# Kernel optimization log

Hardware: AMD Instinct MI355X
Metric: run time of the kernel (lower is better)

Reference implementation:

```python
import jax, jax.numpy as jnp
import numpy as np

THETA = 10000.0


def _apply_rope(xh, positions, theta):
    # xh: [B, H, S, d_k]; positions: [S] int
    d_k = xh.shape[-1]
    inv_freq = theta ** (-jnp.arange(0, d_k, 2, dtype=jnp.float32) / d_k)  # [d_k/2]
    angles = positions.astype(jnp.float32)[:, None] * inv_freq[None, :]     # [S, d_k/2]
    cos = jnp.cos(angles)
    sin = jnp.sin(angles)
    x1 = xh[..., 0::2]
    x2 = xh[..., 1::2]
    r1 = x1 * cos - x2 * sin
    r2 = x1 * sin + x2 * cos
    return jnp.stack([r1, r2], axis=-1).reshape(xh.shape)


def setup_inputs() -> dict:
    key = jax.random.key(0)
    ks = jax.random.split(key, 5)
    B, S, D = 2, 2048, 1024
    std = np.sqrt(1.0 / D).astype(np.float32)
    return {
        "x": jax.random.normal(ks[0], (B, S, D), dtype=jnp.float32),
        "token_positions": jnp.arange(S, dtype=jnp.int64 if jax.config.jax_enable_x64 else jnp.int32),
        "Wq": jax.random.normal(ks[1], (D, D), dtype=jnp.float32) * std,
        "Wk": jax.random.normal(ks[2], (D, D), dtype=jnp.float32) * std,
        "Wv": jax.random.normal(ks[3], (D, D), dtype=jnp.float32) * std,
        "Wo": jax.random.normal(ks[4], (D, D), dtype=jnp.float32) * std,
    }


def reference(x, token_positions, Wq, Wk, Wv, Wo):
    B, S, D = x.shape
    n_heads = 16
    d_k = D // n_heads

    # QKV projections (torch does x @ W.T)
    q = x @ Wq.T
    k = x @ Wk.T
    v = x @ Wv.T

    def split_heads(t):  # [B,S,D] -> [B,H,S,d_k]
        return t.reshape(B, S, n_heads, d_k).transpose(0, 2, 1, 3)

    qh = _apply_rope(split_heads(q), token_positions, THETA)
    kh = _apply_rope(split_heads(k), token_positions, THETA)
    vh = split_heads(v)

    scores = jnp.einsum("bhqd,bhkd->bhqk", qh, kh) / jnp.sqrt(jnp.float32(d_k))
    causal = jnp.tril(jnp.ones((S, S), dtype=bool))
    scores = jnp.where(causal, scores, -jnp.inf)
    attn = jax.nn.softmax(scores, axis=-1)

    out_h = jnp.einsum("bhqk,bhkd->bhqd", attn, vh)  # [B,H,S,d_k]
    out = out_h.transpose(0, 2, 1, 3).reshape(B, S, D)
    return out @ Wo.T
```

## Files before the change

kernel.cpp:

```cpp
#include <hip/hip_runtime.h>

typedef unsigned int u32;
typedef __attribute__((ext_vector_type(8))) short short8;
typedef __attribute__((ext_vector_type(4))) float f32x4;

__device__ __forceinline__ unsigned short f2bf(float f) {
  union { float f; u32 u; } x; x.f = f;
  u32 u = x.u;
  return (unsigned short)((u + 0x7fffu + ((u >> 16) & 1u)) >> 16);
}
__device__ __forceinline__ float bf2f(unsigned short b) {
  union { u32 u; float f; } x; x.u = ((u32)b) << 16;
  return x.f;
}
__device__ __forceinline__ f32x4 mfma_bf16(short8 a, short8 b, f32x4 c) {
  return __builtin_amdgcn_mfma_f32_16x16x32_bf16(a, b, c, 0, 0, 0);
}

typedef __attribute__((address_space(3))) unsigned int lds_u32;
typedef const __attribute__((address_space(1))) unsigned int glb_u32;
__device__ __forceinline__ void gload_lds16(const unsigned short* g, unsigned short* l) {
  __builtin_amdgcn_global_load_lds((glb_u32*)g, (lds_u32*)l, 16, 0, 0);
}

__global__ __launch_bounds__(256) void cvt_kernel(const float* __restrict__ src,
                                                  unsigned short* __restrict__ dst, int n4) {
  int i = blockIdx.x * 256 + threadIdx.x;
  if (i >= n4) return;
  float4 v = ((const float4*)src)[i];
  ushort4 o;
  o.x = f2bf(v.x); o.y = f2bf(v.y); o.z = f2bf(v.z); o.w = f2bf(v.w);
  ((ushort4*)dst)[i] = o;
}

__global__ __launch_bounds__(256) void cvt_w_kernel(const float* __restrict__ wq,
                                                    const float* __restrict__ wk,
                                                    const float* __restrict__ wv,
                                                    const float* __restrict__ wo,
                                                    unsigned short* __restrict__ dqkv,
                                                    unsigned short* __restrict__ dwo) {
  const int i = blockIdx.x * 256 + threadIdx.x;
  const int w = blockIdx.y;
  const float* src = (w == 0) ? wq : (w == 1) ? wk : (w == 2) ? wv : wo;
  unsigned short* dst = (w == 3) ? dwo : dqkv + (size_t)w * 1048576;
  float4 v = ((const float4*)src)[i];
  ushort4 o;
  o.x = f2bf(v.x); o.y = f2bf(v.y); o.z = f2bf(v.z); o.w = f2bf(v.w);
  ((ushort4*)dst)[i] = o;
}

__global__ __launch_bounds__(256) void gemm_qkv(const unsigned short* __restrict__ A,
                                                const unsigned short* __restrict__ B,
                                                unsigned short* __restrict__ qk,
                                                unsigned short* __restrict__ kk,
                                                unsigned short* __restrict__ vtm) {
  constexpr int K = 1024;
  __shared__ unsigned short As[128 * 64];
  __shared__ unsigned short Bs[128 * 64];
  const int tid = threadIdx.x;
  const int wave = tid >> 6, lane = tid & 63;
  const int l15 = lane & 15, quad = lane >> 4;
  const int wr = wave >> 1, wc = wave & 1;
  const int m0 = blockIdx.y * 128, n0 = blockIdx.x * 128;
  f32x4 acc[4][4] = {};
  const int srow = wave * 32 + (lane >> 3);
  const int scol = (((lane & 7) ^ ((lane >> 3) & 7)) * 8);
  const unsigned short* Ag = A + (size_t)(m0 + srow) * K + scol;
  const unsigned short* Bg = B + (size_t)(n0 + srow) * K + scol;
  const int sw0 = ((0 + quad) ^ (l15 & 7)) * 8;
  const int sw1 = ((4 + quad) ^ (l15 & 7)) * 8;
  for (int k0 = 0; k0 < K; k0 += 64) {
    __syncthreads();
#pragma unroll
    for (int r = 0; r < 4; ++r) {
      gload_lds16(Ag + k0 + (size_t)(8 * r) * K, &As[(wave * 32 + 8 * r) * 64]);
      gload_lds16(Bg + k0 + (size_t)(8 * r) * K, &Bs[(wave * 32 + 8 * r) * 64]);
    }
    __syncthreads();
    short8 a[4][2], b[4][2];
#pragma unroll
    for (int i = 0; i < 4; ++i) {
      const int row = (wr * 64 + i * 16 + l15) * 64;
      a[i][0] = *(const short8*)&As[row + sw0];
      a[i][1] = *(const short8*)&As[row + sw1];
    }
#pragma unroll
    for (int j = 0; j < 4; ++j) {
      const int row = (wc * 64 + j * 16 + l15) * 64;
      b[j][0] = *(const short8*)&Bs[row + sw0];
      b[j][1] = *(const short8*)&Bs[row + sw1];
    }
#pragma unroll
    for (int i = 0; i < 4; ++i)
#pragma unroll
      for (int j = 0; j < 4; ++j) {
        acc[i][j] = mfma_bf16(a[i][0], b[j][0], acc[i][j]);
        acc[i][j] = mfma_bf16(a[i][1], b[j][1], acc[i][j]);
      }
  }
  const int proj = n0 >> 10;
  const int nn0 = (n0 & 1023) + wc * 64;
  if (proj < 2) {
    unsigned short* dst = (proj == 0) ? qk : kk;
#pragma unroll
    for (int i = 0; i < 4; ++i) {
      const int mb = m0 + wr * 64 + i * 16 + quad * 4;
#pragma unroll
      for (int j = 0; j < 4; ++j) {
        const int nn = nn0 + j * 16 + l15;
#pragma unroll
        for (int r = 0; r < 4; ++r) dst[(size_t)(mb + r) * 1024 + nn] = f2bf(acc[i][j][r]);
      }
    }
  } else {
#pragma unroll
    for (int i = 0; i < 4; ++i) {
      const int mb = m0 + wr * 64 + i * 16 + quad * 4;
      const int bb = mb >> 11, s = mb & 2047;
#pragma unroll
      for (int j = 0; j < 4; ++j) {
        const int nn = nn0 + j * 16 + l15;
        const int h = nn >> 6, d = nn & 63;
        ushort4 v4;
        v4.x = f2bf(acc[i][j][0]); v4.y = f2bf(acc[i][j][1]);
        v4.z = f2bf(acc[i][j][2]); v4.w = f2bf(acc[i][j][3]);
        *(ushort4*)&vtm[(((size_t)bb * 16 + h) * 64 + d) * 2048 + s] = v4;
      }
    }
  }
}

__global__ __launch_bounds__(256) void rope_kernel(unsigned short* __restrict__ q,
                                                   unsigned short* __restrict__ k,
                                                   const int* __restrict__ pos) {
  const int idx = blockIdx.x * 256 + threadIdx.x;
  const int i = idx & 31;
  const int h = (idx >> 5) & 15;
  const int s = (idx >> 9) & 2047;
  const int b = idx >> 20;
  const float p = (float)pos[s];
  const float inv = exp2f(-0.4152410118609203f * (float)i);
  float sn, cs;
  sincosf(p * inv, &sn, &cs);
  const size_t base = ((size_t)(b * 2048 + s)) * 1024 + h * 64 + 2 * i;
  {
    u32* qp = (u32*)(q + base);
    u32 w = *qp;
    float x1 = bf2f((unsigned short)(w & 0xffff)), x2 = bf2f((unsigned short)(w >> 16));
    *qp = (u32)f2bf(x1 * cs - x2 * sn) | ((u32)f2bf(x1 * sn + x2 * cs) << 16);
  }
  {
    u32* kp = (u32*)(k + base);
    u32 w = *kp;
    float x1 = bf2f((unsigned short)(w & 0xffff)), x2 = bf2f((unsigned short)(w >> 16));
    *kp = (u32)f2bf(x1 * cs - x2 * sn) | ((u32)f2bf(x1 * sn + x2 * cs) << 16);
  }
}

__global__ __launch_bounds__(256) void attn_shared(const unsigned short* __restrict__ qk,
                                                   const unsigned short* __restrict__ kk,
                                                   const unsigned short* __restrict__ vtm,
                                                   unsigned short* __restrict__ om) {
  __shared__ unsigned short Ks[64 * 64];
  __shared__ unsigned short Vs[64 * 64];
  __shared__ u32 PTb[4][2][16 * 36];
  const int tid = threadIdx.x;
  const int wave = tid >> 6, lane = tid & 63;
  const int l15 = lane & 15, quad = lane >> 4;
  u32* PT0 = &PTb[wave][0][0];
  u32* PT1 = &PTb[wave][1][0];
  const int bid = blockIdx.x;
  const int bh = bid & 31;
  const int qblk = 15 - (bid >> 5);
  const int b = bh >> 4, h = bh & 15;
  const int qbase = qblk * 128 + wave * 32;
  const unsigned short* Qp = qk + (size_t)b * 2048 * 1024 + h * 64;
  const unsigned short* Kp = kk + (size_t)b * 2048 * 1024 + h * 64;
  const unsigned short* Vp = vtm + (size_t)bh * 64 * 2048;
  short8 qf[2][2];
#pragma unroll
  for (int f = 0; f < 2; ++f)
#pragma unroll
    for (int hh = 0; hh < 2; ++hh)
      qf[f][hh] = *(const short8*)(Qp + (size_t)(qbase + f * 16 + l15) * 1024 + hh * 32 + quad * 8);
  f32x4 o4[2][4] = {};
  f32x4 ls[2] = {};
  short8 ones;
#pragma unroll
  for (int j = 0; j < 8; ++j) ones[j] = (short)0x3F80;
  const float SC = 0.18033688011112042f;
  const int nkb = (qblk * 128 + 191) >> 6;
  const int nkw = (qbase + 95) >> 6;
  const int srow = wave * 16 + (lane >> 3);
  const int scs = (((lane & 7) ^ (srow & 7)) * 8);
  const unsigned short* KgB = Kp + (size_t)srow * 1024 + scs;
  const unsigned short* VgB = Vp + (size_t)srow * 2048 + scs;
  unsigned short* Kl0 = &Ks[(wave * 16) * 64];
  unsigned short* Kl1 = &Ks[(wave * 16 + 8) * 64];
  unsigned short* Vl0 = &Vs[(wave * 16) * 64];
  unsigned short* Vl1 = &Vs[(wave * 16 + 8) * 64];
  const int sw0 = ((quad ^ (l15 & 7)) * 8);
  const int sw1 = (((4 + quad) ^ (l15 & 7)) * 8);
  for (int kt = 0; kt < nkb; ++kt) {
    const int kbase = kt << 6;
    __syncthreads();
    gload_lds16(KgB + (size_t)kbase * 1024, Kl0);
    gload_lds16(KgB + (size_t)kbase * 1024 + 8 * 1024, Kl1);
    gload_lds16(VgB + kbase, Vl0);
    gload_lds16(VgB + kbase + 8 * 2048, Vl1);
    __syncthreads();
    if (kt < nkw) {
      short8 kb[4][2], vb[4][2];
#pragma unroll
      for (int nt = 0; nt < 4; ++nt) {
        kb[nt][0] = *(const short8*)&Ks[(nt * 16 + l15) * 64 + sw0];
        kb[nt][1] = *(const short8*)&Ks[(nt * 16 + l15) * 64 + sw1];
      }
#pragma unroll
      for (int t = 0; t < 4; ++t) {
        vb[t][0] = *(const short8*)&Vs[(t * 16 + l15) * 64 + sw0];
        vb[t][1] = *(const short8*)&Vs[(t * 16 + l15) * 64 + sw1];
      }
      f32x4 s4[2][4] = {};
#pragma unroll
      for (int f = 0; f < 2; ++f)
#pragma unroll
        for (int nt = 0; nt < 4; ++nt) {
          s4[f][nt] = mfma_bf16(kb[nt][0], qf[f][0], s4[f][nt]);
          s4[f][nt] = mfma_bf16(kb[nt][1], qf[f][1], s4[f][nt]);
        }
      const bool edge = (kbase + 63 > qbase);
#pragma unroll
      for (int f = 0; f < 2; ++f) {
        const int qrow = qbase + f * 16 + l15;
        u32* PTf = f ? PT1 : PT0;
#pragma unroll
        for (int nt = 0; nt < 4; ++nt) {
          const int kv0 = kbase + nt * 16 + quad * 4;
          float p0 = exp2f(s4[f][nt][0] * SC);
          float p1 = exp2f(s4[f][nt][1] * SC);
          float p2 = exp2f(s4[f][nt][2] * SC);
          float p3 = exp2f(s4[f][nt][3] * SC);
          if (edge) {
            if (kv0 > qrow) p0 = 0.f;
            if (kv0 + 1 > qrow) p1 = 0.f;
            if (kv0 + 2 > qrow) p2 = 0.f;
            if (kv0 + 3 > qrow) p3 = 0.f;
          }
          uint2 w;
          w.x = (u32)f2bf(p0) | ((u32)f2bf(p1) << 16);
          w.y = (u32)f2bf(p2) | ((u32)f2bf(p3) << 16);
          *(uint2*)&PTf[l15 * 36 + nt * 8 + quad * 2] = w;
        }
      }
      short8 pa[2][2];
#pragma unroll
      for (int f = 0; f < 2; ++f) {
        const u32* PTf = f ? PT1 : PT0;
#pragma unroll
        for (int hh = 0; hh < 2; ++hh)
          pa[f][hh] = *(const short8*)&PTf[l15 * 36 + hh * 16 + quad * 4];
      }
#pragma unroll
      for (int f = 0; f < 2; ++f) {
#pragma unroll
        for (int t = 0; t < 4; ++t) {
          o4[f][t] = mfma_bf16(pa[f][0], vb[t][0], o4[f][t]);
          o4[f][t] = mfma_bf16(pa[f][1], vb[t][1], o4[f][t]);
        }
        ls[f] = mfma_bf16(pa[f][0], ones, ls[f]);
        ls[f] = mfma_bf16(pa[f][1], ones, ls[f]);
      }
    }
  }
#pragma unroll
  for (int f = 0; f < 2; ++f) {
    f32x4 rl;
#pragma unroll
    for (int r = 0; r < 4; ++r) rl[r] = 1.f / ls[f][r];
#pragma unroll
    for (int t = 0; t < 4; ++t)
#pragma unroll
      for (int r = 0; r < 4; ++r) {
        const int srw = qbase + f * 16 + quad * 4 + r;
        om[((size_t)b * 2048 + srw) * 1024 + h * 64 + t * 16 + l15] = f2bf(o4[f][t][r] * rl[r]);
      }
  }
}

__global__ __launch_bounds__(256) void gemm_out(const unsigned short* __restrict__ A,
                                                const unsigned short* __restrict__ B,
                                                float* __restrict__ C) {
  constexpr int K = 1024;
  __shared__ unsigned short As[64 * 64];
  __shared__ unsigned short Bs[128 * 64];
  const int tid = threadIdx.x;
  const int wave = tid >> 6, lane = tid & 63;
  const int l15 = lane & 15, quad = lane >> 4;
  const int m0 = blockIdx.y * 64, n0 = blockIdx.x * 128;
  f32x4 acc[4][2] = {};
  const int lr = lane >> 3;
  const int scol = (((lane & 7) ^ (lr & 7)) * 8);
  const unsigned short* Ag = A + (size_t)(m0 + wave * 16 + lr) * K + scol;
  const unsigned short* Bg = B + (size_t)(n0 + wave * 32 + lr) * K + scol;
  const int sw0 = ((0 + quad) ^ (l15 & 7)) * 8;
  const int sw1 = ((4 + quad) ^ (l15 & 7)) * 8;
  for (int k0 = 0; k0 < K; k0 += 64) {
    __syncthreads();
    gload_lds16(Ag + k0, &As[(wave * 16) * 64]);
    gload_lds16(Ag + k0 + (size_t)8 * K, &As[(wave * 16 + 8) * 64]);
#pragma unroll
    for (int r = 0; r < 4; ++r)
      gload_lds16(Bg + k0 + (size_t)(8 * r) * K, &Bs[(wave * 32 + 8 * r) * 64]);
    __syncthreads();
    short8 a[4][2], b[2][2];
#pragma unroll
    for (int i = 0; i < 4; ++i) {
      const int row = (i * 16 + l15) * 64;
      a[i][0] = *(const short8*)&As[row + sw0];
      a[i][1] = *(const short8*)&As[row + sw1];
    }
#pragma unroll
    for (int j = 0; j < 2; ++j) {
      const int row = (wave * 32 + j * 16 + l15) * 64;
      b[j][0] = *(const short8*)&Bs[row + sw0];
      b[j][1] = *(const short8*)&Bs[row + sw1];
    }
#pragma unroll
    for (int i = 0; i < 4; ++i)
#pragma unroll
      for (int j = 0; j < 2; ++j) {
        acc[i][j] = mfma_bf16(a[i][0], b[j][0], acc[i][j]);
        acc[i][j] = mfma_bf16(a[i][1], b[j][1], acc[i][j]);
      }
  }
#pragma unroll
  for (int i = 0; i < 4; ++i)
#pragma unroll
    for (int j = 0; j < 2; ++j)
#pragma unroll
      for (int r = 0; r < 4; ++r)
        C[(size_t)(m0 + i * 16 + quad * 4 + r) * 1024 + n0 + wave * 32 + j * 16 + l15] =
            acc[i][j][r];
}

extern "C" void kernel_launch(void* const* d_in, const int* in_sizes, int n_in,
                              void* d_out, int out_size, void* d_ws, size_t ws_size,
                              hipStream_t stream) {
  const float* x  = (const float*)d_in[0];
  const int* pos  = (const int*)d_in[1];
  const float* Wq = (const float*)d_in[2];
  const float* Wk = (const float*)d_in[3];
  const float* Wv = (const float*)d_in[4];
  const float* Wo = (const float*)d_in[5];
  float* out = (float*)d_out;
  char* ws = (char*)d_ws;
  unsigned short* xb   = (unsigned short*)(ws);
  unsigned short* wqkv = (unsigned short*)(ws + (size_t)( 8 << 20));
  unsigned short* wob  = (unsigned short*)(ws + (size_t)(14 << 20));
  unsigned short* qkb  = (unsigned short*)(ws + (size_t)(16 << 20));
  unsigned short* kkb  = (unsigned short*)(ws + (size_t)(24 << 20));
  unsigned short* vtm  = (unsigned short*)(ws + (size_t)(32 << 20));
  unsigned short* om   = (unsigned short*)(ws + (size_t)(40 << 20));

  const int NX4 = 4096 * 1024 / 4;
  hipLaunchKernelGGL(cvt_kernel, dim3(NX4 / 256), dim3(256), 0, stream, x, xb, NX4);
  hipLaunchKernelGGL(cvt_w_kernel, dim3(1024, 4), dim3(256), 0, stream, Wq, Wk, Wv, Wo, wqkv, wob);

  hipLaunchKernelGGL(gemm_qkv, dim3(24, 32), dim3(256), 0, stream, xb, wqkv, qkb, kkb, vtm);
  hipLaunchKernelGGL(rope_kernel, dim3(8192), dim3(256), 0, stream, qkb, kkb, pos);
  hipLaunchKernelGGL(attn_shared, dim3(512), dim3(256), 0, stream, qkb, kkb, vtm, om);
  hipLaunchKernelGGL(gemm_out, dim3(8, 64), dim3(256), 0, stream, om, wob, out);
}
```

Before: 216.3 us.

## Double-buffer K/V tiles in attention with async prefetch of next block

Splits the K and V shared-memory tiles into two buffers and issues the global-to-LDS loads for the next key block before computing on the current one. A partial vmcnt wait plus raw barriers replace the two full syncthreads per iteration. The goal is to hide global load latency behind the MFMA work, at the cost of doubled LDS for K/V, which may lower occupancy. On the last iteration the same block is loaded again redundantly.

```diff
diff --git a/kernel.cpp b/kernel.cpp
--- a/kernel.cpp
+++ b/kernel.cpp
@@ -161,8 +161,8 @@
                                                    const unsigned short* __restrict__ kk,
                                                    const unsigned short* __restrict__ vtm,
                                                    unsigned short* __restrict__ om) {
-  __shared__ unsigned short Ks[64 * 64];
-  __shared__ unsigned short Vs[64 * 64];
+  __shared__ unsigned short Ks[2][64 * 64];
+  __shared__ unsigned short Vs[2][64 * 64];
   __shared__ u32 PTb[4][2][16 * 36];
   const int tid = threadIdx.x;
   const int wave = tid >> 6, lane = tid & 63;
@@ -195,31 +195,38 @@
   const int scs = (((lane & 7) ^ (srow & 7)) * 8);
   const unsigned short* KgB = Kp + (size_t)srow * 1024 + scs;
   const unsigned short* VgB = Vp + (size_t)srow * 2048 + scs;
-  unsigned short* Kl0 = &Ks[(wave * 16) * 64];
-  unsigned short* Kl1 = &Ks[(wave * 16 + 8) * 64];
-  unsigned short* Vl0 = &Vs[(wave * 16) * 64];
-  unsigned short* Vl1 = &Vs[(wave * 16 + 8) * 64];
+  const int l0 = (wave * 16) * 64;
+  const int l1 = (wave * 16 + 8) * 64;
   const int sw0 = ((quad ^ (l15 & 7)) * 8);
   const int sw1 = (((4 + quad) ^ (l15 & 7)) * 8);
+#define ATTN_STAGE(c, kb)                                              \
+  do {                                                                 \
+    gload_lds16(KgB + (size_t)(kb) * 1024, &Ks[c][l0]);                \
+    gload_lds16(KgB + (size_t)(kb) * 1024 + 8 * 1024, &Ks[c][l1]);     \
+    gload_lds16(VgB + (kb), &Vs[c][l0]);                               \
+    gload_lds16(VgB + (kb) + 8 * 2048, &Vs[c][l1]);                    \
+  } while (0)
+  ATTN_STAGE(0, 0);
+  int cur = 0;
   for (int kt = 0; kt < nkb; ++kt) {
-    const int kbase = kt << 6;
-    __syncthreads();
-    gload_lds16(KgB + (size_t)kbase * 1024, Kl0);
-    gload_lds16(KgB + (size_t)kbase * 1024 + 8 * 1024, Kl1);
-    gload_lds16(VgB + kbase, Vl0);
-    gload_lds16(VgB + kbase + 8 * 2048, Vl1);
-    __syncthreads();
+    __builtin_amdgcn_s_barrier();
+    const int knext = (kt + 1 < nkb ? kt + 1 : kt) << 6;
+    ATTN_STAGE(cur ^ 1, knext);
+    asm volatile("s_waitcnt vmcnt(4)" ::: "memory");
+    __builtin_amdgcn_s_barrier();
+    __builtin_amdgcn_sched_barrier(0);
     if (kt < nkw) {
+      const int kbase = kt << 6;
       short8 kb[4][2], vb[4][2];
 #pragma unroll
       for (int nt = 0; nt < 4; ++nt) {
-        kb[nt][0] = *(const short8*)&Ks[(nt * 16 + l15) * 64 + sw0];
-        kb[nt][1] = *(const short8*)&Ks[(nt * 16 + l15) * 64 + sw1];
+        kb[nt][0] = *(const short8*)&Ks[cur][(nt * 16 + l15) * 64 + sw0];
+        kb[nt][1] = *(const short8*)&Ks[cur][(nt * 16 + l15) * 64 + sw1];
       }
 #pragma unroll
       for (int t = 0; t < 4; ++t) {
-        vb[t][0] = *(const short8*)&Vs[(t * 16 + l15) * 64 + sw0];
-        vb[t][1] = *(const short8*)&Vs[(t * 16 + l15) * 64 + sw1];
+        vb[t][0] = *(const short8*)&Vs[cur][(t * 16 + l15) * 64 + sw0];
+        vb[t][1] = *(const short8*)&Vs[cur][(t * 16 + l15) * 64 + sw1];
       }
       f32x4 s4[2][4] = {};
 #pragma unroll
@@ -272,7 +279,9 @@
         ls[f] = mfma_bf16(pa[f][1], ones, ls[f]);
       }
     }
-  }
+    cur ^= 1;
+  }
+#undef ATTN_STAGE
 #pragma unroll
   for (int f = 0; f < 2; ++f) {
     f32x4 rl;
```

Result: no change. 214.9 us (-0.7%).
